# Performance work log

Measured on AMD Instinct MI355X. Metric: run time of the kernel, lower is better.

The kernel has to match this reference:

```python
import jax, jax.numpy as jnp
import numpy as np

N_NODES = 10000
N_EDGES = 100000
D = 248        # algebra_dim (E8)
H = 512        # hidden_dim of update MLP
NNZ = 2480     # nonzero structure-constant triples (~10 per basis element)
LN_EPS = 1e-5


def setup_inputs() -> dict:
    key = jax.random.key(0)
    ks = jax.random.split(key, 12)
    features = jax.random.normal(ks[0], (N_NODES, D), dtype=jnp.float32)
    edge_index = jax.random.randint(ks[1], (2, N_EDGES), 0, N_NODES, dtype=jnp.int32)
    # Linear weights (torch convention: y = x @ W.T + b)
    W_msg = jax.random.normal(ks[2], (D, D), dtype=jnp.float32) / np.sqrt(D)
    W1 = jax.random.normal(ks[3], (H, D), dtype=jnp.float32) / np.sqrt(D)
    b1 = jnp.zeros((H,), dtype=jnp.float32)
    W2 = jax.random.normal(ks[4], (D, H), dtype=jnp.float32) / np.sqrt(H)
    b2 = jnp.zeros((D,), dtype=jnp.float32)
    gamma = jnp.ones((D,), dtype=jnp.float32)
    beta = jnp.zeros((D,), dtype=jnp.float32)
    # Sparse Lie-bracket structure constants: bracket(x, y)[K_t] += C_t * x[I_t] * y[J_t]
    I = jax.random.randint(ks[5], (NNZ,), 0, D, dtype=jnp.int32)
    J = jax.random.randint(ks[6], (NNZ,), 0, D, dtype=jnp.int32)
    K = jax.random.randint(ks[7], (NNZ,), 0, D, dtype=jnp.int32)
    C = jax.random.normal(ks[8], (NNZ,), dtype=jnp.float32) * 0.1
    return {"features": features, "edge_index": edge_index, "W_msg": W_msg,
            "W1": W1, "b1": b1, "W2": W2, "b2": b2,
            "gamma": gamma, "beta": beta, "I": I, "J": J, "K": K, "C": C}


def _layer_norm(x, gamma, beta):
    mu = jnp.mean(x, axis=-1, keepdims=True)
    xc = x - mu
    var = jnp.mean(xc * xc, axis=-1, keepdims=True)
    return xc * jax.lax.rsqrt(var + LN_EPS) * gamma + beta


def reference(features, edge_index, W_msg, W1, b1, W2, b2, gamma, beta, I, J, K, C):
    src, tgt = edge_index[0], edge_index[1]
    src_proj = features[src] @ W_msg.T           # (E, D) edge gather + linear
    tgt_feats = features[tgt]                    # (E, D)
    # sparse Lie bracket: out[e, K_t] += C_t * src_proj[e, I_t] * tgt_feats[e, J_t]
    prod = src_proj[:, I] * tgt_feats[:, J] * C  # (E, NNZ)
    messages = jnp.zeros((src.shape[0], D), features.dtype).at[:, K].add(prod)
    # scatter-add messages onto target nodes
    agg = jax.ops.segment_sum(messages, tgt, num_segments=N_NODES)  # (N, D)
    # residual MLP update + LayerNorm
    h = jax.nn.silu(agg @ W1.T + b1) @ W2.T + b2
    return _layer_norm(features + h, gamma, beta)
```

## Files before the change

### kernel.cpp

```cpp
#include <hip/hip_runtime.h>
#include <hip/hip_fp16.h>

#define N_NODES 10000
#define N_EDGES 100000
#define D 248
#define DP 256
#define HDIM 512
#define NNZ 2480
#define LN_EPS 1e-5f
#define PAD_ROWS 128
#define NTHR 256
#define CAP 32

typedef __attribute__((ext_vector_type(8))) _Float16 f16x8_t;
typedef __attribute__((ext_vector_type(4))) float f32x4_t;

__device__ __forceinline__ unsigned short f2h(float f) {
  return __builtin_bit_cast(unsigned short, __float2half(f));
}
__device__ __forceinline__ unsigned packh2(float a, float b) {
  return __builtin_bit_cast(unsigned, __floats2half2_rn(a, b));
}
__device__ __forceinline__ void gload_lds16(const unsigned short* gp,
                                            unsigned short* lds_base) {
  __builtin_amdgcn_global_load_lds(
      (const __attribute__((address_space(1))) void*)gp,
      (__attribute__((address_space(3))) void*)lds_base, 16, 0, 0);
}

__device__ __forceinline__ void cast_row_dev(const float* src, unsigned short* dst,
                                             int r, int sr, int sc, int dc) {
  for (int c = threadIdx.x; c < dc; c += NTHR) {
    float v = (r < sr && c < sc) ? src[(size_t)r * sc + c] : 0.f;
    dst[(size_t)r * dc + c] = f2h(v);
  }
}

#define U_FEAT 1250
#define U_WM (U_FEAT + DP)
#define U_W1 (U_WM + HDIM)
#define U_W2 (U_W1 + DP)
#define U_CSR (U_W2 + 1)
#define HIST_U ((N_EDGES + 255) / 256)
#define U_TOTAL (U_CSR + HIST_U)

__global__ __launch_bounds__(NTHR) void prep_kernel(
    const float* __restrict__ features, const float* __restrict__ W_msg,
    const float* __restrict__ W1, const float* __restrict__ W2,
    const int* __restrict__ ei,
    unsigned short* __restrict__ featH, unsigned short* __restrict__ WmH,
    unsigned short* __restrict__ W1H, unsigned short* __restrict__ W2H,
    const int* __restrict__ Iv, const int* __restrict__ Jv,
    const int* __restrict__ Kv, const float* __restrict__ Cv,
    int* __restrict__ rsK, int2* __restrict__ trip,
    int* __restrict__ deg, int* __restrict__ ovfc,
    int* __restrict__ esrc, int2* __restrict__ ovf) {
  const int u = blockIdx.x;
  const int tid = threadIdx.x;
  if (u < U_FEAT) {
    const int r = u * 8 + (tid >> 5);
    const int c = tid & 31;
    uint4 o = make_uint4(0u, 0u, 0u, 0u);
    if (c < 31) {
      const float* src = features + (size_t)r * D + c * 8;
      float4 v0 = *(const float4*)(src);
      float4 v1 = *(const float4*)(src + 4);
      o.x = packh2(v0.x, v0.y);
      o.y = packh2(v0.z, v0.w);
      o.z = packh2(v1.x, v1.y);
      o.w = packh2(v1.z, v1.w);
    }
    *(uint4*)(featH + (size_t)r * DP + c * 8) = o;
  } else if (u < U_WM) {
    cast_row_dev(W_msg, WmH, u - U_FEAT, D, D, DP);
  } else if (u < U_W1) {
    cast_row_dev(W1, W1H, u - U_WM, HDIM, D, DP);
  } else if (u < U_W2) {
    cast_row_dev(W2, W2H, u - U_W1, D, HDIM, HDIM);
  } else if (u < U_CSR) {
    __shared__ int cnt[D];
    __shared__ int off[D];
    for (int k = tid; k < D; k += NTHR) cnt[k] = 0;
    __syncthreads();
    for (int t = tid; t < NNZ; t += NTHR) atomicAdd(&cnt[Kv[t]], 1);
    __syncthreads();
    if (tid == 0) {
      int run = 0;
      for (int k = 0; k < D; k++) { off[k] = run; rsK[k] = run; run += cnt[k]; }
      rsK[D] = run;
    }
    __syncthreads();
    for (int t = tid; t < NNZ; t += NTHR) {
      int pos = atomicAdd(&off[Kv[t]], 1);
      trip[pos] = make_int2((Jv[t] << 16) | Iv[t], __float_as_int(Cv[t]));
    }
  } else {
    int e = (u - U_CSR) * 256 + tid;
    if (e < N_EDGES) {
      int src = ei[e];
      int tgt = ei[N_EDGES + e];
      int r = atomicAdd(&deg[tgt], 1);
      if (r < CAP) {
        esrc[tgt * CAP + r] = src;
      } else {
        int o = atomicAdd(ovfc, 1);
        ovf[o] = make_int2(tgt, src);
      }
    }
  }
}

template <int EPI>
__device__ __forceinline__ void gemm_tile(
    const unsigned short* __restrict__ A, const unsigned short* __restrict__ B,
    const float* __restrict__ bias, void* __restrict__ Cout,
    int M, int ncl2, int K, int lda, int ldb, int ldc, int tile,
    unsigned short* As, unsigned short* Bs) {
  const int tid = threadIdx.x;
  const int wave = tid >> 6;
  const int lane = tid & 63;
  const int wm = wave >> 1;
  const int wn = wave & 1;
  const int ml = lane & 15;
  const int q = lane >> 4;
  const int srow = lane >> 3;
  const int sg = lane & 7;
  const int sgs = sg ^ srow;
  const int ncol = 1 << ncl2;
  const int n0 = (tile & (ncol - 1)) << 6;
  const int m0 = (tile >> ncl2) << 6;

  f32x4_t acc[2][2];
#pragma unroll
  for (int i = 0; i < 2; i++)
#pragma unroll
    for (int j = 0; j < 2; j++) acc[i][j] = (f32x4_t)0.f;

  for (int k0 = 0; k0 < K; k0 += 64) {
#pragma unroll
    for (int i = 0; i < 2; i++) {
      int t = wave * 2 + i;
      gload_lds16(A + (size_t)(m0 + t * 8 + srow) * lda + k0 + sgs * 8, As + t * 512);
    }
#pragma unroll
    for (int i = 0; i < 2; i++) {
      int t = wave * 2 + i;
      gload_lds16(B + (size_t)(n0 + t * 8 + srow) * ldb + k0 + sgs * 8, Bs + t * 512);
    }
    __syncthreads();
#pragma unroll
    for (int kk = 0; kk < 2; kk++) {
      f16x8_t a[2], b[2];
#pragma unroll
      for (int im = 0; im < 2; im++) {
        int row = wm * 32 + im * 16 + ml;
        int c8 = (kk * 4 + q) ^ (row & 7);
        a[im] = *(const f16x8_t*)(As + row * 64 + c8 * 8);
      }
#pragma unroll
      for (int jn = 0; jn < 2; jn++) {
        int row = wn * 32 + jn * 16 + ml;
        int c8 = (kk * 4 + q) ^ (row & 7);
        b[jn] = *(const f16x8_t*)(Bs + row * 64 + c8 * 8);
      }
#pragma unroll
      for (int im = 0; im < 2; im++)
#pragma unroll
        for (int jn = 0; jn < 2; jn++)
          acc[im][jn] = __builtin_amdgcn_mfma_f32_16x16x32_f16(
              a[im], b[jn], acc[im][jn], 0, 0, 0);
    }
    __syncthreads();
  }

#pragma unroll
  for (int im = 0; im < 2; im++) {
#pragma unroll
    for (int jn = 0; jn < 2; jn++) {
      int gn = n0 + wn * 32 + jn * 16 + ml;
#pragma unroll
      for (int reg = 0; reg < 4; reg++) {
        int gm = m0 + wm * 32 + im * 16 + q * 4 + reg;
        if (gm >= M) continue;
        float v = acc[im][jn][reg];
        if (EPI == 0) {
          ((unsigned short*)Cout)[(size_t)gm * ldc + gn] = f2h(v);
        } else if (EPI == 1) {
          v += bias[gn];
          v = v / (1.f + __expf(-v));
          ((unsigned short*)Cout)[(size_t)gm * ldc + gn] = f2h(v);
        } else {
          v += (gn < D) ? bias[gn] : 0.f;
          ((float*)Cout)[(size_t)gm * ldc + gn] = v;
        }
      }
    }
  }
}

template <int EPI>
__global__ __launch_bounds__(NTHR) void gemm_kernel(
    const unsigned short* __restrict__ A, const unsigned short* __restrict__ B,
    const float* __restrict__ bias, void* __restrict__ Cout,
    int M, int ncl2, int K, int lda, int ldb, int ldc) {
  __shared__ unsigned short As[64 * 64];
  __shared__ unsigned short Bs[64 * 64];
  gemm_tile<EPI>(A, B, bias, Cout, M, ncl2, K, lda, ldb, ldc, blockIdx.x, As, Bs);
}

__global__ __launch_bounds__(NTHR) void gather_bracket(
    const unsigned short* __restrict__ S2H, const unsigned short* __restrict__ FH,
    const int* __restrict__ deg, const int* __restrict__ esrc,
    const int* __restrict__ ovfc, const int2* __restrict__ ovf,
    const int* __restrict__ rsK, const int2* __restrict__ trip,
    unsigned short* __restrict__ agg) {
  __shared__ unsigned sSg[8][DP / 2];
  __shared__ unsigned sS2[4][DP];
  __shared__ unsigned sF2[4][DP];
  const int tid = threadIdx.x;
  const int lane = tid & 63;
  const int half = lane >> 5;
  const int c = lane & 31;
  const int node8 = tid >> 5;
  const int n = blockIdx.x * 8 + node8;

  {
    const int dg = deg[n];
    const int dc = (dg < CAP) ? dg : CAP;
    int eid = (c < dc) ? esrc[n * CAP + c] : 0;

    __half2 a0 = __floats2half2_rn(0.f, 0.f), a1 = a0, a2 = a0, a3 = a0;
    __half2 b0 = a0, b1 = a0, b2 = a0, b3 = a0;
    const unsigned short* Sc = S2H + (size_t)c * 8;
    int j = 0;
    for (; j + 2 <= dc; j += 2) {
      int s0 = __shfl(eid, half * 32 + j);
      int s1 = __shfl(eid, half * 32 + j + 1);
      uint4 u0 = *(const uint4*)(Sc + (size_t)s0 * DP);
      uint4 u1 = *(const uint4*)(Sc + (size_t)s1 * DP);
      a0 = __hadd2(a0, __builtin_bit_cast(__half2, u0.x));
      a1 = __hadd2(a1, __builtin_bit_cast(__half2, u0.y));
      a2 = __hadd2(a2, __builtin_bit_cast(__half2, u0.z));
      a3 = __hadd2(a3, __builtin_bit_cast(__half2, u0.w));
      b0 = __hadd2(b0, __builtin_bit_cast(__half2, u1.x));
      b1 = __hadd2(b1, __builtin_bit_cast(__half2, u1.y));
      b2 = __hadd2(b2, __builtin_bit_cast(__half2, u1.z));
      b3 = __hadd2(b3, __builtin_bit_cast(__half2, u1.w));
    }
    if (j < dc) {
      int s = __shfl(eid, half * 32 + j);
      uint4 u0 = *(const uint4*)(Sc + (size_t)s * DP);
      a0 = __hadd2(a0, __builtin_bit_cast(__half2, u0.x));
      a1 = __hadd2(a1, __builtin_bit_cast(__half2, u0.y));
      a2 = __hadd2(a2, __builtin_bit_cast(__half2, u0.z));
      a3 = __hadd2(a3, __builtin_bit_cast(__half2, u0.w));
    }
    if (dg > CAP) {
      int novf = *ovfc;
      for (int o = 0; o < novf; o++) {
        int2 e = ovf[o];
        if (e.x == n) {
          uint4 u0 = *(const uint4*)(Sc + (size_t)e.y * DP);
          a0 = __hadd2(a0, __builtin_bit_cast(__half2, u0.x));
          a1 = __hadd2(a1, __builtin_bit_cast(__half2, u0.y));
          a2 = __hadd2(a2, __builtin_bit_cast(__half2, u0.z));
          a3 = __hadd2(a3, __builtin_bit_cast(__half2, u0.w));
        }
      }
    }
    unsigned* d = &sSg[node8][c * 4];
    d[0] = __builtin_bit_cast(unsigned, __hadd2(a0, b0));
    d[1] = __builtin_bit_cast(unsigned, __hadd2(a1, b1));
    d[2] = __builtin_bit_cast(unsigned, __hadd2(a2, b2));
    d[3] = __builtin_bit_cast(unsigned, __hadd2(a3, b3));
  }
  __syncthreads();

  const int wv = tid >> 6;
  const int n0 = blockIdx.x * 8 + wv * 2;
  const int n1 = n0 + 1;
  {
#pragma unroll
    for (int j = 0; j < 4; j++) {
      int k = lane * 4 + j;
      unsigned w0 = sSg[wv * 2][lane * 2 + (j >> 1)];
      unsigned w1 = sSg[wv * 2 + 1][lane * 2 + (j >> 1)];
      unsigned h0 = (j & 1) ? (w0 >> 16) : (w0 & 0xFFFF);
      unsigned h1 = (j & 1) ? (w1 >> 16) : (w1 & 0xFFFF);
      sS2[wv][k] = h0 | (h1 << 16);
    }
    ushort4 u0 = *(const ushort4*)(FH + (size_t)n0 * DP + lane * 4);
    ushort4 u1 = *(const ushort4*)(FH + (size_t)n1 * DP + lane * 4);
    unsigned* d = &sF2[wv][lane * 4];
    d[0] = (unsigned)u0.x | ((unsigned)u1.x << 16);
    d[1] = (unsigned)u0.y | ((unsigned)u1.y << 16);
    d[2] = (unsigned)u0.z | ((unsigned)u1.z << 16);
    d[3] = (unsigned)u0.w | ((unsigned)u1.w << 16);
  }
  __syncthreads();

  const unsigned* S2 = sS2[wv];
  const unsigned* F2 = sF2[wv];
#pragma unroll
  for (int kk = 0; kk < 4; kk++) {
    const int k = lane + kk * 64;
    float a0 = 0.f, a1 = 0.f, b0 = 0.f, b1 = 0.f;
    if (k < D) {
      const int tb = rsK[k], te = rsK[k + 1];
      int t = tb;
      for (; t + 2 <= te; t += 2) {
        int2 t0 = trip[t], t1 = trip[t + 1];
        __half2 p0 = __hmul2(__builtin_bit_cast(__half2, S2[t0.x & 0xFFFF]),
                             __builtin_bit_cast(__half2, F2[t0.x >> 16]));
        __half2 p1 = __hmul2(__builtin_bit_cast(__half2, S2[t1.x & 0xFFFF]),
                             __builtin_bit_cast(__half2, F2[t1.x >> 16]));
        float2 q0 = __half22float2(p0);
        float2 q1 = __half22float2(p1);
        const float c0 = __int_as_float(t0.y), c1 = __int_as_float(t1.y);
        a0 += c0 * q0.x; a1 += c0 * q0.y;
        b0 += c1 * q1.x; b1 += c1 * q1.y;
      }
      if (t < te) {
        int2 t0 = trip[t];
        __half2 p0 = __hmul2(__builtin_bit_cast(__half2, S2[t0.x & 0xFFFF]),
                             __builtin_bit_cast(__half2, F2[t0.x >> 16]));
        float2 q0 = __half22float2(p0);
        const float c0 = __int_as_float(t0.y);
        a0 += c0 * q0.x; a1 += c0 * q0.y;
      }
    }
    agg[(size_t)n0 * DP + k] = f2h(a0 + b0);
    agg[(size_t)n1 * DP + k] = f2h(a1 + b1);
  }
}

__global__ __launch_bounds__(NTHR) void ln_kernel(
    const float* __restrict__ x0, const float* __restrict__ h2,
    const float* __restrict__ gamma, const float* __restrict__ beta,
    float* __restrict__ out) {
  const int tid = threadIdx.x;
  const int wv = tid >> 6;
  const int lane = tid & 63;
  const int n = blockIdx.x * 4 + wv;

  float4 x = make_float4(0.f, 0.f, 0.f, 0.f);
  if (lane < 62) {
    float4 f = *(const float4*)(x0 + (size_t)n * D + lane * 4);
    float4 h = *(const float4*)(h2 + (size_t)n * DP + lane * 4);
    x = make_float4(f.x + h.x, f.y + h.y, f.z + h.z, f.w + h.w);
  }
  float s = x.x + x.y + x.z + x.w;
#pragma unroll
  for (int o = 32; o > 0; o >>= 1) s += __shfl_xor(s, o);
  const float mu = s * (1.f / (float)D);
  float4 xc = make_float4(x.x - mu, x.y - mu, x.z - mu, x.w - mu);
  float v = 0.f;
  if (lane < 62) v = xc.x * xc.x + xc.y * xc.y + xc.z * xc.z + xc.w * xc.w;
#pragma unroll
  for (int o = 32; o > 0; o >>= 1) v += __shfl_xor(v, o);
  const float rstd = rsqrtf(v * (1.f / (float)D) + LN_EPS);
  if (lane < 62) {
    float4 g = *(const float4*)(gamma + lane * 4);
    float4 b = *(const float4*)(beta + lane * 4);
    float4 o;
    o.x = xc.x * rstd * g.x + b.x;
    o.y = xc.y * rstd * g.y + b.y;
    o.z = xc.z * rstd * g.z + b.z;
    o.w = xc.w * rstd * g.w + b.w;
    *(float4*)(out + (size_t)n * D + lane * 4) = o;
  }
}

extern "C" void kernel_launch(void* const* d_in, const int* in_sizes, int n_in,
                              void* d_out, int out_size, void* d_ws, size_t ws_size,
                              hipStream_t stream) {
  const float* features = (const float*)d_in[0];
  const int*   ei       = (const int*)d_in[1];
  const float* W_msg    = (const float*)d_in[2];
  const float* W1       = (const float*)d_in[3];
  const float* b1       = (const float*)d_in[4];
  const float* W2       = (const float*)d_in[5];
  const float* b2       = (const float*)d_in[6];
  const float* gamma    = (const float*)d_in[7];
  const float* beta     = (const float*)d_in[8];
  const int*   Iv       = (const int*)d_in[9];
  const int*   Jv       = (const int*)d_in[10];
  const int*   Kv       = (const int*)d_in[11];
  const float* Cv       = (const float*)d_in[12];
  float* out = (float*)d_out;

  char* cur = (char*)d_ws;
  auto alloc = [&](size_t bytes) {
    char* p = cur;
    cur += (bytes + 255) & ~(size_t)255;
    return p;
  };
  const size_t NP = (size_t)N_NODES + PAD_ROWS;
  unsigned short* featH = (unsigned short*)alloc(NP * DP * 2);
  unsigned short* WmH   = (unsigned short*)alloc((size_t)DP * DP * 2);
  unsigned short* W1H   = (unsigned short*)alloc((size_t)HDIM * DP * 2);
  unsigned short* W2H   = (unsigned short*)alloc((size_t)DP * HDIM * 2);
  unsigned short* S2H   = (unsigned short*)alloc(NP * DP * 2);
  unsigned short* aggH  = (unsigned short*)alloc(NP * DP * 2);
  unsigned short* H1H   = (unsigned short*)alloc(NP * HDIM * 2);
  float*          H2    = (float*)alloc((size_t)N_NODES * DP * 4);
  int*  rsK  = (int*)alloc((D + 1) * 4);
  int2* trip = (int2*)alloc(NNZ * 8);
  int*  deg  = (int*)alloc((N_NODES + 64) * 4);
  int*  ovfc = deg + N_NODES;
  int*  esrc = (int*)alloc((size_t)N_NODES * CAP * 4);
  int2* ovf  = (int2*)alloc((size_t)N_EDGES * 8);

  dim3 blk(NTHR);

  hipMemsetAsync(deg, 0, (size_t)(N_NODES + 1) * 4, stream);
  prep_kernel<<<U_TOTAL, blk, 0, stream>>>(
      features, W_msg, W1, W2, ei, featH, WmH, W1H, W2H,
      Iv, Jv, Kv, Cv, rsK, trip, deg, ovfc, esrc, ovf);
  gemm_kernel<0><<<157 * 4, blk, 0, stream>>>(
      featH, WmH, nullptr, S2H, N_NODES, 2, DP, DP, DP, DP);
  gather_bracket<<<N_NODES / 8, blk, 0, stream>>>(
      S2H, featH, deg, esrc, ovfc, ovf, rsK, trip, aggH);
  gemm_kernel<1><<<157 * 8, blk, 0, stream>>>(
      aggH, W1H, b1, H1H, N_NODES, 3, DP, DP, DP, HDIM);
  gemm_kernel<2><<<157 * 4, blk, 0, stream>>>(
      H1H, W2H, b2, H2, N_NODES, 2, HDIM, HDIM, HDIM, DP);
  ln_kernel<<<N_NODES / 4, blk, 0, stream>>>(features, H2, gamma, beta, out);
}
```

Baseline: 160.2 us.

## Fuse MLP GEMMs, bias, SiLU, residual and LayerNorm into one kernel

Replaces the two MLP GEMM launches and the separate LayerNorm kernel with a single kernel in which each block owns 64 rows. The block computes the hidden activations chunk by chunk in LDS and accumulates the second GEMM in registers before applying the residual and LayerNorm in-register. This removes the global round trips of the fp16 hidden tensor and the fp32 pre-norm tensor, plus two launches. In exchange, only 157 blocks run, with large LDS use and serialized per-block work, which may underfill the GPU.

Result: slower. 192.5 us (+20.1%).

```diff
diff --git a/kernel.cpp b/kernel.cpp
--- a/kernel.cpp
+++ b/kernel.cpp
@@ -11,6 +11,7 @@
 #define PAD_ROWS 128
 #define NTHR 256
 #define CAP 32
+#define PBLK 157
 
 typedef __attribute__((ext_vector_type(8))) _Float16 f16x8_t;
 typedef __attribute__((ext_vector_type(4))) float f32x4_t;
@@ -110,12 +111,12 @@
   }
 }
 
-template <int EPI>
-__device__ __forceinline__ void gemm_tile(
+__global__ __launch_bounds__(NTHR) void gemm_kernel(
     const unsigned short* __restrict__ A, const unsigned short* __restrict__ B,
-    const float* __restrict__ bias, void* __restrict__ Cout,
-    int M, int ncl2, int K, int lda, int ldb, int ldc, int tile,
-    unsigned short* As, unsigned short* Bs) {
+    unsigned short* __restrict__ Cout,
+    int M, int ncl2, int K, int lda, int ldb, int ldc) {
+  __shared__ unsigned short As[64 * 64];
+  __shared__ unsigned short Bs[64 * 64];
   const int tid = threadIdx.x;
   const int wave = tid >> 6;
   const int lane = tid & 63;
@@ -127,6 +128,7 @@
   const int sg = lane & 7;
   const int sgs = sg ^ srow;
   const int ncol = 1 << ncl2;
+  const int tile = blockIdx.x;
   const int n0 = (tile & (ncol - 1)) << 6;
   const int m0 = (tile >> ncl2) << 6;
 
@@ -182,30 +184,10 @@
       for (int reg = 0; reg < 4; reg++) {
         int gm = m0 + wm * 32 + im * 16 + q * 4 + reg;
         if (gm >= M) continue;
-        float v = acc[im][jn][reg];
-        if (EPI == 0) {
-          ((unsigned short*)Cout)[(size_t)gm * ldc + gn] = f2h(v);
-        } else if (EPI == 1) {
-          v += bias[gn];
-          v = v / (1.f + __expf(-v));
-          ((unsigned short*)Cout)[(size_t)gm * ldc + gn] = f2h(v);
-        } else {
-          v += (gn < D) ? bias[gn] : 0.f;
-          ((float*)Cout)[(size_t)gm * ldc + gn] = v;
-        }
-      }
-    }
-  }
-}
-
-template <int EPI>
-__global__ __launch_bounds__(NTHR) void gemm_kernel(
-    const unsigned short* __restrict__ A, const unsigned short* __restrict__ B,
-    const float* __restrict__ bias, void* __restrict__ Cout,
-    int M, int ncl2, int K, int lda, int ldb, int ldc) {
-  __shared__ unsigned short As[64 * 64];
-  __shared__ unsigned short Bs[64 * 64];
-  gemm_tile<EPI>(A, B, bias, Cout, M, ncl2, K, lda, ldb, ldc, blockIdx.x, As, Bs);
+        Cout[(size_t)gm * ldc + gn] = f2h(acc[im][jn][reg]);
+      }
+    }
+  }
 }
 
 __global__ __launch_bounds__(NTHR) void gather_bracket(
@@ -334,40 +316,184 @@
   }
 }
 
-__global__ __launch_bounds__(NTHR) void ln_kernel(
-    const float* __restrict__ x0, const float* __restrict__ h2,
+__global__ __launch_bounds__(NTHR) void mlp_ln_kernel(
+    const unsigned short* __restrict__ aggH,
+    const unsigned short* __restrict__ W1H,
+    const unsigned short* __restrict__ W2H,
+    const float* __restrict__ b1, const float* __restrict__ b2,
+    const float* __restrict__ features,
     const float* __restrict__ gamma, const float* __restrict__ beta,
     float* __restrict__ out) {
+  __shared__ unsigned short Ast[64 * 64];
+  __shared__ unsigned short Bst[64 * 64];
+  __shared__ unsigned short Tlds[64 * 64];
+  __shared__ unsigned short W2st[256 * 64];
+  __shared__ float lnp[4][64];
+
   const int tid = threadIdx.x;
   const int wv = tid >> 6;
   const int lane = tid & 63;
-  const int n = blockIdx.x * 4 + wv;
-
-  float4 x = make_float4(0.f, 0.f, 0.f, 0.f);
-  if (lane < 62) {
-    float4 f = *(const float4*)(x0 + (size_t)n * D + lane * 4);
-    float4 h = *(const float4*)(h2 + (size_t)n * DP + lane * 4);
-    x = make_float4(f.x + h.x, f.y + h.y, f.z + h.z, f.w + h.w);
-  }
-  float s = x.x + x.y + x.z + x.w;
-#pragma unroll
-  for (int o = 32; o > 0; o >>= 1) s += __shfl_xor(s, o);
-  const float mu = s * (1.f / (float)D);
-  float4 xc = make_float4(x.x - mu, x.y - mu, x.z - mu, x.w - mu);
-  float v = 0.f;
-  if (lane < 62) v = xc.x * xc.x + xc.y * xc.y + xc.z * xc.z + xc.w * xc.w;
-#pragma unroll
-  for (int o = 32; o > 0; o >>= 1) v += __shfl_xor(v, o);
-  const float rstd = rsqrtf(v * (1.f / (float)D) + LN_EPS);
-  if (lane < 62) {
-    float4 g = *(const float4*)(gamma + lane * 4);
-    float4 b = *(const float4*)(beta + lane * 4);
-    float4 o;
-    o.x = xc.x * rstd * g.x + b.x;
-    o.y = xc.y * rstd * g.y + b.y;
-    o.z = xc.z * rstd * g.z + b.z;
-    o.w = xc.w * rstd * g.w + b.w;
-    *(float4*)(out + (size_t)n * D + lane * 4) = o;
+  const int ml = lane & 15;
+  const int q = lane >> 4;
+  const int srow = lane >> 3;
+  const int sg = lane & 7;
+  const int sgs = sg ^ srow;
+  const int m0 = blockIdx.x * 64;
+
+  f32x4_t h2[4][4];
+#pragma unroll
+  for (int im = 0; im < 4; im++)
+#pragma unroll
+    for (int jn = 0; jn < 4; jn++) h2[im][jn] = (f32x4_t)0.f;
+
+  for (int hb = 0; hb < 8; hb++) {
+    f32x4_t t4[4];
+#pragma unroll
+    for (int jn = 0; jn < 4; jn++) t4[jn] = (f32x4_t)0.f;
+    for (int kb = 0; kb < 4; kb++) {
+#pragma unroll
+      for (int i = 0; i < 2; i++) {
+        int t = wv * 2 + i;
+        gload_lds16(aggH + (size_t)(m0 + t * 8 + srow) * DP + kb * 64 + sgs * 8,
+                    Ast + t * 512);
+      }
+#pragma unroll
+      for (int i = 0; i < 2; i++) {
+        int t = wv * 2 + i;
+        gload_lds16(W1H + (size_t)(hb * 64 + t * 8 + srow) * DP + kb * 64 + sgs * 8,
+                    Bst + t * 512);
+      }
+      __syncthreads();
+#pragma unroll
+      for (int kk = 0; kk < 2; kk++) {
+        const int arow = wv * 16 + ml;
+        f16x8_t a = *(const f16x8_t*)(Ast + arow * 64 + ((kk * 4 + q) ^ (arow & 7)) * 8);
+#pragma unroll
+        for (int jn = 0; jn < 4; jn++) {
+          int brow = jn * 16 + ml;
+          f16x8_t b = *(const f16x8_t*)(Bst + brow * 64 + ((kk * 4 + q) ^ (brow & 7)) * 8);
+          t4[jn] = __builtin_amdgcn_mfma_f32_16x16x32_f16(a, b, t4[jn], 0, 0, 0);
+        }
+      }
+      __syncthreads();
+    }
+#pragma unroll
+    for (int jn = 0; jn < 4; jn++) {
+      const int h = jn * 16 + ml;
+      const float bias = b1[hb * 64 + h];
+#pragma unroll
+      for (int reg = 0; reg < 4; reg++) {
+        float v = t4[jn][reg] + bias;
+        v = v / (1.f + __expf(-v));
+        int m = wv * 16 + q * 4 + reg;
+        int c8 = (h >> 3) ^ (m & 7);
+        Tlds[m * 64 + c8 * 8 + (h & 7)] = f2h(v);
+      }
+    }
+#pragma unroll
+    for (int i = 0; i < 8; i++) {
+      int t = wv * 8 + i;
+      gload_lds16(W2H + (size_t)(t * 8 + srow) * HDIM + hb * 64 + sgs * 8,
+                  W2st + t * 512);
+    }
+    __syncthreads();
+#pragma unroll
+    for (int kk = 0; kk < 2; kk++) {
+      f16x8_t a[4], b[4];
+#pragma unroll
+      for (int im = 0; im < 4; im++) {
+        int r = im * 16 + ml;
+        a[im] = *(const f16x8_t*)(Tlds + r * 64 + ((kk * 4 + q) ^ (r & 7)) * 8);
+      }
+#pragma unroll
+      for (int jn = 0; jn < 4; jn++) {
+        int r = wv * 64 + jn * 16 + ml;
+        b[jn] = *(const f16x8_t*)(W2st + r * 64 + ((kk * 4 + q) ^ (r & 7)) * 8);
+      }
+#pragma unroll
+      for (int im = 0; im < 4; im++)
+#pragma unroll
+        for (int jn = 0; jn < 4; jn++)
+          h2[im][jn] = __builtin_amdgcn_mfma_f32_16x16x32_f16(
+              a[im], b[jn], h2[im][jn], 0, 0, 0);
+    }
+    __syncthreads();
+  }
+
+  float mu[4][4], rstd[4][4];
+#pragma unroll
+  for (int im = 0; im < 4; im++) {
+#pragma unroll
+    for (int reg = 0; reg < 4; reg++) {
+      const int gm = m0 + im * 16 + q * 4 + reg;
+      float s = 0.f;
+#pragma unroll
+      for (int jn = 0; jn < 4; jn++) {
+        const int col = wv * 64 + jn * 16 + ml;
+        float x = 0.f;
+        if (col < D && gm < N_NODES)
+          x = h2[im][jn][reg] + b2[col] + features[(size_t)gm * D + col];
+        h2[im][jn][reg] = x;
+        s += x;
+      }
+#pragma unroll
+      for (int o = 8; o > 0; o >>= 1) s += __shfl_xor(s, o);
+      if (ml == 0) lnp[wv][im * 16 + q * 4 + reg] = s;
+    }
+  }
+  __syncthreads();
+#pragma unroll
+  for (int im = 0; im < 4; im++)
+#pragma unroll
+    for (int reg = 0; reg < 4; reg++) {
+      int r = im * 16 + q * 4 + reg;
+      mu[im][reg] = (lnp[0][r] + lnp[1][r] + lnp[2][r] + lnp[3][r]) * (1.f / (float)D);
+    }
+  __syncthreads();
+#pragma unroll
+  for (int im = 0; im < 4; im++) {
+#pragma unroll
+    for (int reg = 0; reg < 4; reg++) {
+      const int gm = m0 + im * 16 + q * 4 + reg;
+      float ss = 0.f;
+#pragma unroll
+      for (int jn = 0; jn < 4; jn++) {
+        const int col = wv * 64 + jn * 16 + ml;
+        if (col < D && gm < N_NODES) {
+          float xc = h2[im][jn][reg] - mu[im][reg];
+          ss += xc * xc;
+        }
+      }
+#pragma unroll
+      for (int o = 8; o > 0; o >>= 1) ss += __shfl_xor(ss, o);
+      if (ml == 0) lnp[wv][im * 16 + q * 4 + reg] = ss;
+    }
+  }
+  __syncthreads();
+#pragma unroll
+  for (int im = 0; im < 4; im++)
+#pragma unroll
+    for (int reg = 0; reg < 4; reg++) {
+      int r = im * 16 + q * 4 + reg;
+      float var = (lnp[0][r] + lnp[1][r] + lnp[2][r] + lnp[3][r]) * (1.f / (float)D);
+      rstd[im][reg] = rsqrtf(var + LN_EPS);
+    }
+#pragma unroll
+  for (int im = 0; im < 4; im++) {
+#pragma unroll
+    for (int jn = 0; jn < 4; jn++) {
+      const int col = wv * 64 + jn * 16 + ml;
+      if (col >= D) continue;
+      const float g = gamma[col];
+      const float bt = beta[col];
+#pragma unroll
+      for (int reg = 0; reg < 4; reg++) {
+        const int gm = m0 + im * 16 + q * 4 + reg;
+        if (gm < N_NODES)
+          out[(size_t)gm * D + col] =
+              (h2[im][jn][reg] - mu[im][reg]) * rstd[im][reg] * g + bt;
+      }
+    }
   }
 }
 
@@ -402,8 +528,6 @@
   unsigned short* W2H   = (unsigned short*)alloc((size_t)DP * HDIM * 2);
   unsigned short* S2H   = (unsigned short*)alloc(NP * DP * 2);
   unsigned short* aggH  = (unsigned short*)alloc(NP * DP * 2);
-  unsigned short* H1H   = (unsigned short*)alloc(NP * HDIM * 2);
-  float*          H2    = (float*)alloc((size_t)N_NODES * DP * 4);
   int*  rsK  = (int*)alloc((D + 1) * 4);
   int2* trip = (int2*)alloc(NNZ * 8);
   int*  deg  = (int*)alloc((N_NODES + 64) * 4);
@@ -417,13 +541,10 @@
   prep_kernel<<<U_TOTAL, blk, 0, stream>>>(
       features, W_msg, W1, W2, ei, featH, WmH, W1H, W2H,
       Iv, Jv, Kv, Cv, rsK, trip, deg, ovfc, esrc, ovf);
-  gemm_kernel<0><<<157 * 4, blk, 0, stream>>>(
-      featH, WmH, nullptr, S2H, N_NODES, 2, DP, DP, DP, DP);
+  gemm_kernel<<<PBLK * 4, blk, 0, stream>>>(
+      featH, WmH, S2H, N_NODES, 2, DP, DP, DP, DP);
   gather_bracket<<<N_NODES / 8, blk, 0, stream>>>(
       S2H, featH, deg, esrc, ovfc, ovf, rsK, trip, aggH);
-  gemm_kernel<1><<<157 * 8, blk, 0, stream>>>(
-      aggH, W1H, b1, H1H, N_NODES, 3, DP, DP, DP, HDIM);
-  gemm_kernel<2><<<157 * 4, blk, 0, stream>>>(
-      H1H, W2H, b2, H2, N_NODES, 2, HDIM, HDIM, HDIM, DP);
-  ln_kernel<<<N_NODES / 4, blk, 0, stream>>>(features, H2, gamma, beta, out);
-}
+  mlp_ln_kernel<<<PBLK, blk, 0, stream>>>(
+      aggH, W1H, W2H, b1, b2, features, gamma, beta, out);
+}
```

## Fuse message-projection GEMM into prep kernel with on-the-fly fp32-to-fp16 casting

Applied to the files above, without the earlier changes.

The first GEMM (features @ W_msg^T) now runs inside the prep kernel as extra blocks. Each block reads fp32 features and W_msg directly, converts them to fp16 into swizzled LDS tiles, and computes S2H. This removes one kernel launch and the separate W_msg cast buffer, and lets the GEMM overlap with the other prep work. In exchange the GEMM loads fp32 through registers instead of async global-to-LDS loads, so each tile's global traffic roughly doubles.

After: 162.6 us. No clear change (+1.5%).

```diff
diff --git a/kernel.cpp b/kernel.cpp
--- a/kernel.cpp
+++ b/kernel.cpp
@@ -11,6 +11,7 @@
 #define PAD_ROWS 128
 #define NTHR 256
 #define CAP 32
+#define PBLK 157
 
 typedef __attribute__((ext_vector_type(8))) _Float16 f16x8_t;
 typedef __attribute__((ext_vector_type(4))) float f32x4_t;
@@ -36,29 +37,116 @@
   }
 }
 
-#define U_FEAT 1250
-#define U_WM (U_FEAT + DP)
-#define U_W1 (U_WM + HDIM)
-#define U_W2 (U_W1 + DP)
-#define U_CSR (U_W2 + 1)
+#define G1U 628
+#define UF_END (G1U + 1250)
+#define UW1_END (UF_END + 512)
+#define UW2_END (UW1_END + 256)
+#define UCSR_END (UW2_END + 1)
 #define HIST_U ((N_EDGES + 255) / 256)
-#define U_TOTAL (U_CSR + HIST_U)
-
-__global__ __launch_bounds__(NTHR) void prep_kernel(
+#define FRONT_BLOCKS (UCSR_END + HIST_U)
+
+__global__ __launch_bounds__(NTHR) void front_kernel(
     const float* __restrict__ features, const float* __restrict__ W_msg,
     const float* __restrict__ W1, const float* __restrict__ W2,
     const int* __restrict__ ei,
-    unsigned short* __restrict__ featH, unsigned short* __restrict__ WmH,
-    unsigned short* __restrict__ W1H, unsigned short* __restrict__ W2H,
+    unsigned short* __restrict__ featH, unsigned short* __restrict__ W1H,
+    unsigned short* __restrict__ W2H, unsigned short* __restrict__ S2H,
     const int* __restrict__ Iv, const int* __restrict__ Jv,
     const int* __restrict__ Kv, const float* __restrict__ Cv,
     int* __restrict__ rsK, int2* __restrict__ trip,
     int* __restrict__ deg, int* __restrict__ ovfc,
     int* __restrict__ esrc, int2* __restrict__ ovf) {
+  __shared__ union {
+    struct { unsigned short As[4096]; unsigned short Bs[4096]; } g;
+    struct { int cnt[D]; int off[D]; } csr;
+  } sm;
   const int u = blockIdx.x;
   const int tid = threadIdx.x;
-  if (u < U_FEAT) {
-    const int r = u * 8 + (tid >> 5);
+
+  if (u < G1U) {
+    const int wave = tid >> 6;
+    const int lane = tid & 63;
+    const int wm = wave >> 1;
+    const int wn = wave & 1;
+    const int ml = lane & 15;
+    const int q = lane >> 4;
+    const int sr = tid >> 3;
+    const int scg = tid & 7;
+    const int n0 = (u & 3) << 6;
+    const int m0 = (u >> 2) << 6;
+
+    f32x4_t acc[2][2];
+#pragma unroll
+    for (int i = 0; i < 2; i++)
+#pragma unroll
+      for (int j = 0; j < 2; j++) acc[i][j] = (f32x4_t)0.f;
+
+    for (int kb = 0; kb < 4; kb++) {
+      const int g8 = kb * 8 + scg;
+#pragma unroll
+      for (int r2 = 0; r2 < 2; r2++) {
+        const int row = r2 * 32 + sr;
+        uint4 o = make_uint4(0u, 0u, 0u, 0u);
+        if (m0 + row < N_NODES && g8 < 31) {
+          const float* p = features + (size_t)(m0 + row) * D + g8 * 8;
+          float4 v0 = *(const float4*)p;
+          float4 v1 = *(const float4*)(p + 4);
+          o.x = packh2(v0.x, v0.y); o.y = packh2(v0.z, v0.w);
+          o.z = packh2(v1.x, v1.y); o.w = packh2(v1.z, v1.w);
+        }
+        *(uint4*)(sm.g.As + row * 64 + (scg ^ (row & 7)) * 8) = o;
+      }
+#pragma unroll
+      for (int r2 = 0; r2 < 2; r2++) {
+        const int row = r2 * 32 + sr;
+        uint4 o = make_uint4(0u, 0u, 0u, 0u);
+        if (n0 + row < D && g8 < 31) {
+          const float* p = W_msg + (size_t)(n0 + row) * D + g8 * 8;
+          float4 v0 = *(const float4*)p;
+          float4 v1 = *(const float4*)(p + 4);
+          o.x = packh2(v0.x, v0.y); o.y = packh2(v0.z, v0.w);
+          o.z = packh2(v1.x, v1.y); o.w = packh2(v1.z, v1.w);
+        }
+        *(uint4*)(sm.g.Bs + row * 64 + (scg ^ (row & 7)) * 8) = o;
+      }
+      __syncthreads();
+#pragma unroll
+      for (int kk = 0; kk < 2; kk++) {
+        f16x8_t a[2], b[2];
+#pragma unroll
+        for (int im = 0; im < 2; im++) {
+          int row = wm * 32 + im * 16 + ml;
+          a[im] = *(const f16x8_t*)(sm.g.As + row * 64 + ((kk * 4 + q) ^ (row & 7)) * 8);
+        }
+#pragma unroll
+        for (int jn = 0; jn < 2; jn++) {
+          int row = wn * 32 + jn * 16 + ml;
+          b[jn] = *(const f16x8_t*)(sm.g.Bs + row * 64 + ((kk * 4 + q) ^ (row & 7)) * 8);
+        }
+#pragma unroll
+        for (int im = 0; im < 2; im++)
+#pragma unroll
+          for (int jn = 0; jn < 2; jn++)
+            acc[im][jn] = __builtin_amdgcn_mfma_f32_16x16x32_f16(
+                a[im], b[jn], acc[im][jn], 0, 0, 0);
+      }
+      __syncthreads();
+    }
+#pragma unroll
+    for (int im = 0; im < 2; im++) {
+#pragma unroll
+      for (int jn = 0; jn < 2; jn++) {
+        int gn = n0 + wn * 32 + jn * 16 + ml;
+#pragma unroll
+        for (int reg = 0; reg < 4; reg++) {
+          int gm = m0 + wm * 32 + im * 16 + q * 4 + reg;
+          if (gm < N_NODES)
+            S2H[(size_t)gm * DP + gn] = f2h(acc[im][jn][reg]);
+        }
+      }
+    }
+  } else if (u < UF_END) {
+    const int r = (u - G1U) * 8 + (tid >> 5);
     const int c = tid & 31;
     uint4 o = make_uint4(0u, 0u, 0u, 0u);
     if (c < 31) {
@@ -71,31 +159,27 @@
       o.w = packh2(v1.z, v1.w);
     }
     *(uint4*)(featH + (size_t)r * DP + c * 8) = o;
-  } else if (u < U_WM) {
-    cast_row_dev(W_msg, WmH, u - U_FEAT, D, D, DP);
-  } else if (u < U_W1) {
-    cast_row_dev(W1, W1H, u - U_WM, HDIM, D, DP);
-  } else if (u < U_W2) {
-    cast_row_dev(W2, W2H, u - U_W1, D, HDIM, HDIM);
-  } else if (u < U_CSR) {
-    __shared__ int cnt[D];
-    __shared__ int off[D];
-    for (int k = tid; k < D; k += NTHR) cnt[k] = 0;
+  } else if (u < UW1_END) {
+    cast_row_dev(W1, W1H, u - UF_END, HDIM, D, DP);
+  } else if (u < UW2_END) {
+    cast_row_dev(W2, W2H, u - UW1_END, D, HDIM, HDIM);
+  } else if (u < UCSR_END) {
+    for (int k = tid; k < D; k += NTHR) sm.csr.cnt[k] = 0;
     __syncthreads();
-    for (int t = tid; t < NNZ; t += NTHR) atomicAdd(&cnt[Kv[t]], 1);
+    for (int t = tid; t < NNZ; t += NTHR) atomicAdd(&sm.csr.cnt[Kv[t]], 1);
     __syncthreads();
     if (tid == 0) {
       int run = 0;
-      for (int k = 0; k < D; k++) { off[k] = run; rsK[k] = run; run += cnt[k]; }
+      for (int k = 0; k < D; k++) { sm.csr.off[k] = run; rsK[k] = run; run += sm.csr.cnt[k]; }
       rsK[D] = run;
     }
     __syncthreads();
     for (int t = tid; t < NNZ; t += NTHR) {
-      int pos = atomicAdd(&off[Kv[t]], 1);
+      int pos = atomicAdd(&sm.csr.off[Kv[t]], 1);
       trip[pos] = make_int2((Jv[t] << 16) | Iv[t], __float_as_int(Cv[t]));
     }
   } else {
-    int e = (u - U_CSR) * 256 + tid;
+    int e = (u - UCSR_END) * 256 + tid;
     if (e < N_EDGES) {
       int src = ei[e];
       int tgt = ei[N_EDGES + e];
@@ -111,11 +195,12 @@
 }
 
 template <int EPI>
-__device__ __forceinline__ void gemm_tile(
+__global__ __launch_bounds__(NTHR) void gemm_kernel(
     const unsigned short* __restrict__ A, const unsigned short* __restrict__ B,
     const float* __restrict__ bias, void* __restrict__ Cout,
-    int M, int ncl2, int K, int lda, int ldb, int ldc, int tile,
-    unsigned short* As, unsigned short* Bs) {
+    int M, int ncl2, int K, int lda, int ldb, int ldc) {
+  __shared__ unsigned short As[64 * 64];
+  __shared__ unsigned short Bs[64 * 64];
   const int tid = threadIdx.x;
   const int wave = tid >> 6;
   const int lane = tid & 63;
@@ -127,6 +212,7 @@
   const int sg = lane & 7;
   const int sgs = sg ^ srow;
   const int ncol = 1 << ncl2;
+  const int tile = blockIdx.x;
   const int n0 = (tile & (ncol - 1)) << 6;
   const int m0 = (tile >> ncl2) << 6;
 
@@ -183,9 +269,7 @@
         int gm = m0 + wm * 32 + im * 16 + q * 4 + reg;
         if (gm >= M) continue;
         float v = acc[im][jn][reg];
-        if (EPI == 0) {
-          ((unsigned short*)Cout)[(size_t)gm * ldc + gn] = f2h(v);
-        } else if (EPI == 1) {
+        if (EPI == 1) {
           v += bias[gn];
           v = v / (1.f + __expf(-v));
           ((unsigned short*)Cout)[(size_t)gm * ldc + gn] = f2h(v);
@@ -196,16 +280,6 @@
       }
     }
   }
-}
-
-template <int EPI>
-__global__ __launch_bounds__(NTHR) void gemm_kernel(
-    const unsigned short* __restrict__ A, const unsigned short* __restrict__ B,
-    const float* __restrict__ bias, void* __restrict__ Cout,
-    int M, int ncl2, int K, int lda, int ldb, int ldc) {
-  __shared__ unsigned short As[64 * 64];
-  __shared__ unsigned short Bs[64 * 64];
-  gemm_tile<EPI>(A, B, bias, Cout, M, ncl2, K, lda, ldb, ldc, blockIdx.x, As, Bs);
 }
 
 __global__ __launch_bounds__(NTHR) void gather_bracket(
@@ -397,7 +471,6 @@
   };
   const size_t NP = (size_t)N_NODES + PAD_ROWS;
   unsigned short* featH = (unsigned short*)alloc(NP * DP * 2);
-  unsigned short* WmH   = (unsigned short*)alloc((size_t)DP * DP * 2);
   unsigned short* W1H   = (unsigned short*)alloc((size_t)HDIM * DP * 2);
   unsigned short* W2H   = (unsigned short*)alloc((size_t)DP * HDIM * 2);
   unsigned short* S2H   = (unsigned short*)alloc(NP * DP * 2);
@@ -414,16 +487,14 @@
   dim3 blk(NTHR);
 
   hipMemsetAsync(deg, 0, (size_t)(N_NODES + 1) * 4, stream);
-  prep_kernel<<<U_TOTAL, blk, 0, stream>>>(
-      features, W_msg, W1, W2, ei, featH, WmH, W1H, W2H,
+  front_kernel<<<FRONT_BLOCKS, blk, 0, stream>>>(
+      features, W_msg, W1, W2, ei, featH, W1H, W2H, S2H,
       Iv, Jv, Kv, Cv, rsK, trip, deg, ovfc, esrc, ovf);
-  gemm_kernel<0><<<157 * 4, blk, 0, stream>>>(
-      featH, WmH, nullptr, S2H, N_NODES, 2, DP, DP, DP, DP);
   gather_bracket<<<N_NODES / 8, blk, 0, stream>>>(
       S2H, featH, deg, esrc, ovfc, ovf, rsK, trip, aggH);
-  gemm_kernel<1><<<157 * 8, blk, 0, stream>>>(
+  gemm_kernel<1><<<PBLK * 8, blk, 0, stream>>>(
       aggH, W1H, b1, H1H, N_NODES, 3, DP, DP, DP, HDIM);
-  gemm_kernel<2><<<157 * 4, blk, 0, stream>>>(
+  gemm_kernel<2><<<PBLK * 4, blk, 0, stream>>>(
       H1H, W2H, b2, H2, N_NODES, 2, HDIM, HDIM, HDIM, DP);
   ln_kernel<<<N_NODES / 4, blk, 0, stream>>>(features, H2, gamma, beta, out);
 }
```
